# Kernel tuning notes

Hardware: AMD Instinct MI355X
Metric: run time of the kernel (lower is better)

Reference implementation:

```python
import jax, jax.numpy as jnp
import numpy as np

D_MODEL = 1024
N_HEADS = 16
SEQ = 2048
BATCH = 2
EPS = 1e-5


def layer_norm(x, g, b):
    mu = jnp.mean(x, axis=-1, keepdims=True)
    var = jnp.mean(jnp.square(x - mu), axis=-1, keepdims=True)
    return (x - mu) * jax.lax.rsqrt(var + EPS) * g + b


def setup_inputs() -> dict:
    key = jax.random.key(0)
    ks = jax.random.split(key, 10)
    D = D_MODEL
    s = lambda fan_in: 1.0 / np.sqrt(fan_in)
    return {
        "x": jax.random.normal(ks[0], (BATCH, SEQ, D), dtype=jnp.float32),
        # weights stored [in, out] (torch Linear is y = x @ W.T; equivalent math)
        "w_attn": jax.random.uniform(ks[1], (D, 3 * D), minval=-s(D), maxval=s(D), dtype=jnp.float32),
        "b_attn": jnp.zeros((3 * D,), jnp.float32),
        "w_proj": jax.random.uniform(ks[2], (D, D), minval=-s(D), maxval=s(D), dtype=jnp.float32),
        "b_proj": jnp.zeros((D,), jnp.float32),
        "ln1_g": jnp.ones((D,), jnp.float32),
        "ln1_b": jnp.zeros((D,), jnp.float32),
        "ln2_g": jnp.ones((D,), jnp.float32),
        "ln2_b": jnp.zeros((D,), jnp.float32),
        "w_fc1": jax.random.uniform(ks[3], (D, 4 * D), minval=-s(D), maxval=s(D), dtype=jnp.float32),
        "b_fc1": jnp.zeros((4 * D,), jnp.float32),
        "w_fc2": jax.random.uniform(ks[4], (4 * D, D), minval=-s(4 * D), maxval=s(4 * D), dtype=jnp.float32),
        "b_fc2": jnp.zeros((D,), jnp.float32),
    }


def reference(x, w_attn, b_attn, w_proj, b_proj, ln1_g, ln1_b, ln2_g, ln2_b, w_fc1, b_fc1, w_fc2, b_fc2):
    B, L, D = x.shape
    H = N_HEADS
    Dh = D // H

    # --- attention sublayer ---
    h = layer_norm(x, ln1_g, ln1_b)
    qkv = h @ w_attn + b_attn                      # [B, L, 3D]
    # SOURCE BUG (faithful): q, k, v are all taken from the k third.
    k = qkv[..., D:2 * D]
    kh = k.reshape(B, L, H, Dh).transpose(0, 2, 1, 3)   # [B, H, L, Dh]
    att = jnp.einsum('bhqd,bhkd->bhqk', kh, kh) / jnp.sqrt(jnp.float32(Dh))
    att = jax.nn.softmax(att, axis=-1)
    out = jnp.einsum('bhqk,bhkd->bhqd', att, kh)         # [B, H, L, Dh]
    out = out.transpose(0, 2, 1, 3).reshape(B, L, D)
    x = x + (out @ w_proj + b_proj)

    # --- feed-forward sublayer ---
    h = layer_norm(x, ln2_g, ln2_b)
    h = jax.nn.relu(h @ w_fc1 + b_fc1)
    x = x + (h @ w_fc2 + b_fc2)
    return x
```

## Files before the change

kernel.cpp:

```cpp
#include <hip/hip_runtime.h>


typedef __attribute__((ext_vector_type(8))) short s8v;
typedef __attribute__((ext_vector_type(4))) short s4v;
typedef __attribute__((ext_vector_type(4))) float f4v;

#define D_MODEL 1024
#define SEQ 2048
#define BATCH 2
#define NH 16
#define DH 64
#define MROWS (BATCH * SEQ)

#define KH_SCALE 0.42466088f
#define KH_ISCALE 2.3548200f

__device__ __forceinline__ float b2f(unsigned short u) {
  union { unsigned int i; float f; } v; v.i = ((unsigned int)u) << 16; return v.f;
}
__device__ __forceinline__ unsigned short f2b(float f) {
  unsigned int i = __builtin_bit_cast(unsigned int, f);
  unsigned int r = (i + 0x7fffu + ((i >> 16) & 1u)) >> 16;
  return (unsigned short)r;
}
__device__ __forceinline__ void async16(const void* g, void* l) {
  __builtin_amdgcn_global_load_lds(
      (const __attribute__((address_space(1))) unsigned int*)g,
      (__attribute__((address_space(3))) unsigned int*)l, 16, 0, 0);
}
__device__ __forceinline__ unsigned short cvt_b(float f) { return f2b(f); }
__device__ __forceinline__ unsigned short cvt_b(unsigned short u) { return u; }

__device__ __forceinline__ float xp2(float x) {
#if __has_builtin(__builtin_amdgcn_exp2f)
  return __builtin_amdgcn_exp2f(x);
#else
  return exp2f(x);
#endif
}

__device__ __forceinline__ s4v cvt4(float a, float b, float c, float d) {
  unsigned int lo, hi;
  asm("v_cvt_pk_bf16_f32 %0, %1, %2" : "=v"(lo) : "v"(a), "v"(b));
  asm("v_cvt_pk_bf16_f32 %0, %1, %2" : "=v"(hi) : "v"(c), "v"(d));
  union { unsigned long long u; s4v v; } u;
  u.u = ((unsigned long long)hi << 32) | (unsigned long long)lo;
  return u.v;
}

#if __has_builtin(__builtin_amdgcn_mfma_f32_16x16x16_bf16)
__device__ __forceinline__ f4v mfma16(s4v a, s4v b, f4v c) {
  return __builtin_amdgcn_mfma_f32_16x16x16_bf16(a, b, c, 0, 0, 0);
}
#elif __has_builtin(__builtin_amdgcn_mfma_f32_16x16x16bf16_1k)
__device__ __forceinline__ f4v mfma16(s4v a, s4v b, f4v c) {
  return __builtin_amdgcn_mfma_f32_16x16x16bf16_1k(a, b, c, 0, 0, 0);
}
#else
__device__ __forceinline__ f4v mfma16(s4v a, s4v b, f4v c) {
  s8v aa = {a[0], a[1], a[2], a[3], 0, 0, 0, 0};
  s8v bb = {b[0], b[1], b[2], b[3], 0, 0, 0, 0};
  return __builtin_amdgcn_mfma_f32_16x16x32_bf16(aa, bb, c, 0, 0, 0);
}
#endif

typedef __attribute__((address_space(3))) const unsigned short* lds_cp;
__device__ __forceinline__ s4v tr16(lds_cp p) {
  unsigned long long d;
  asm volatile("ds_read_b64_tr_b16 %0, %1" : "=v"(d) : "v"(p));
  return __builtin_bit_cast(s4v, d);
}

__device__ __forceinline__ int xcd_swz(int bidl, int nwg) {
  return (nwg & 7) ? bidl : ((bidl & 7) * (nwg >> 3) + (bidl >> 3));
}

__global__ __launch_bounds__(256) void ln_kernel(
    const float* __restrict__ x, const float* __restrict__ g,
    const float* __restrict__ bb, unsigned short* __restrict__ out) {
  int row = blockIdx.x;
  int t = threadIdx.x;
  const float* xr = x + (size_t)row * D_MODEL;
  float v[4];
  float s = 0.f, s2 = 0.f;
#pragma unroll
  for (int i = 0; i < 4; ++i) {
    float f = xr[t + 256 * i];
    v[i] = f; s += f; s2 += f * f;
  }
#pragma unroll
  for (int off = 1; off < 64; off <<= 1) {
    s += __shfl_xor(s, off, 64);
    s2 += __shfl_xor(s2, off, 64);
  }
  __shared__ float red[8];
  if ((t & 63) == 0) { red[t >> 6] = s; red[4 + (t >> 6)] = s2; }
  __syncthreads();
  s = red[0] + red[1] + red[2] + red[3];
  s2 = red[4] + red[5] + red[6] + red[7];
  float mu = s * (1.f / D_MODEL);
  float var = s2 * (1.f / D_MODEL) - mu * mu;
  float rstd = rsqrtf(var + 1e-5f);
#pragma unroll
  for (int i = 0; i < 4; ++i) {
    int c = t + 256 * i;
    float h = (v[i] - mu) * rstd * g[c] + bb[c];
    out[(size_t)row * D_MODEL + c] = f2b(h);
  }
}

template <typename T>
__global__ __launch_bounds__(256) void transpose_b(
    const T* __restrict__ src, unsigned short* __restrict__ dst,
    int srcStride, int dstStride, long long srcBatch, long long dstBatch) {
  __shared__ unsigned short tile[64][65];
  const T* s = src + (size_t)blockIdx.z * srcBatch;
  unsigned short* d = dst + (size_t)blockIdx.z * dstBatch;
  int n0 = blockIdx.x * 64, k0 = blockIdx.y * 64;
  for (int i = threadIdx.x; i < 4096; i += 256) {
    int k = i >> 6, n = i & 63;
    tile[k][n] = cvt_b(s[(size_t)(k0 + k) * srcStride + n0 + n]);
  }
  __syncthreads();
  for (int i = threadIdx.x; i < 4096; i += 256) {
    int n = i >> 6, k = i & 63;
    d[(size_t)(n0 + n) * dstStride + k0 + k] = tile[k][n];
  }
}

template <int RES, bool RELU, bool KH, int OUTF, int BM, int BN>
__global__ __launch_bounds__(256) void gemm_bt(
    const unsigned short* __restrict__ A, const unsigned short* __restrict__ Bt,
    const float* __restrict__ bias, const float* __restrict__ res,
    void* __restrict__ out, int M, int N, int K) {
  constexpr int MT = BM / 32;
  constexpr int NT = BN / 32;
  __shared__ __align__(16) unsigned short lsA[2][BM * 64];
  __shared__ __align__(16) unsigned short lsB[2][BN * 64];
  int tid = threadIdx.x;
  int lane = tid & 63, w = tid >> 6, quad = lane >> 4, l16 = lane & 15;
  int bidl = blockIdx.y * (int)gridDim.x + blockIdx.x;
  int swz = xcd_swz(bidl, (int)(gridDim.x * gridDim.y));
  int m0 = (swz / (int)gridDim.x) * BM, n0 = (swz % (int)gridDim.x) * BN;
  int wm = (w >> 1) * (BM / 2), wn = (w & 1) * (BN / 2);
  f4v acc[MT][NT] = {};

  auto stage = [&](int bsel, int ktE) {
#pragma unroll
    for (int i = 0; i < MT; ++i) {
      int cb = w * (BM * 2) + i * 64;
      int ci = cb + lane;
      int row = ci >> 3, c = ci & 7;
      int cs = c ^ (row & 7);
      async16(A + (size_t)(m0 + row) * K + ktE + cs * 8, &lsA[bsel][cb * 8]);
    }
#pragma unroll
    for (int i = 0; i < NT; ++i) {
      int cb = w * (BN * 2) + i * 64;
      int ci = cb + lane;
      int row = ci >> 3, c = ci & 7;
      int cs = c ^ (row & 7);
      async16(Bt + (size_t)(n0 + row) * K + ktE + cs * 8, &lsB[bsel][cb * 8]);
    }
  };

  stage(0, 0);
  int nK = K >> 6;
  for (int kt = 0; kt < nK; ++kt) {
    int b = kt & 1;
    if (kt + 1 < nK) {
      stage(b ^ 1, (kt + 1) << 6);
      if constexpr (MT + NT == 4)      asm volatile("s_waitcnt vmcnt(4)" ::: "memory");
      else if constexpr (MT + NT == 6) asm volatile("s_waitcnt vmcnt(6)" ::: "memory");
      else                             asm volatile("s_waitcnt vmcnt(8)" ::: "memory");
    } else {
      asm volatile("s_waitcnt vmcnt(0)" ::: "memory");
    }
    __builtin_amdgcn_sched_barrier(0);
    __builtin_amdgcn_s_barrier();
    __builtin_amdgcn_sched_barrier(0);
#pragma unroll
    for (int s = 0; s < 2; ++s) {
      s8v af[MT], bf[NT];
#pragma unroll
      for (int t = 0; t < MT; ++t) {
        int am = wm + t * 16 + l16;
        int ac = (s * 4 + quad) ^ (am & 7);
        af[t] = *(const s8v*)(&lsA[b][am * 64 + ac * 8]);
      }
#pragma unroll
      for (int t = 0; t < NT; ++t) {
        int bn = wn + t * 16 + l16;
        int bc = (s * 4 + quad) ^ (bn & 7);
        bf[t] = *(const s8v*)(&lsB[b][bn * 64 + bc * 8]);
      }
#pragma unroll
      for (int ti = 0; ti < MT; ++ti)
#pragma unroll
        for (int tj = 0; tj < NT; ++tj)
          acc[ti][tj] = __builtin_amdgcn_mfma_f32_16x16x32_bf16(
              af[ti], bf[tj], acc[ti][tj], 0, 0, 0);
    }
    asm volatile("s_waitcnt lgkmcnt(0)" ::: "memory");
    __builtin_amdgcn_sched_barrier(0);
    __builtin_amdgcn_s_barrier();
    __builtin_amdgcn_sched_barrier(0);
  }
#pragma unroll
  for (int tj = 0; tj < NT; ++tj) {
    int col = n0 + wn + tj * 16 + l16;
    float bv = bias[col];
#pragma unroll
    for (int ti = 0; ti < MT; ++ti) {
#pragma unroll
      for (int r = 0; r < 4; ++r) {
        int rowg = m0 + wm + ti * 16 + quad * 4 + r;
        float vv = acc[ti][tj][r] + bv;
        if (KH) vv *= KH_SCALE;
        if (RES == 2) vv += res[(size_t)rowg * N + col];
        if (RELU) vv = fmaxf(vv, 0.f);
        size_t oidx;
        if (KH) {
          int b2 = rowg >> 11, l = rowg & 2047, h = col >> 6, d = col & 63;
          oidx = (((size_t)(b2 * NH + h)) * SEQ + l) * DH + d;
        } else {
          oidx = (size_t)rowg * N + col;
        }
        if (OUTF == 0) ((unsigned short*)out)[oidx] = f2b(vv);
        else           ((float*)out)[oidx] = vv;
      }
    }
  }
}

__global__ __launch_bounds__(512, 2) void gemm256(
    const unsigned short* __restrict__ A, const unsigned short* __restrict__ Bt,
    const float* __restrict__ bias, unsigned short* __restrict__ out,
    bool relu, int M, int N, int K) {
  __shared__ __align__(16) unsigned short lsA[2][2][128 * 64];
  __shared__ __align__(16) unsigned short lsB[2][2][128 * 64];
  int tid = threadIdx.x;
  int lane = tid & 63, w = tid >> 6, quad = lane >> 4, l16 = lane & 15;
  int wr = w >> 2, wc = w & 3;
  int bidl = blockIdx.y * (int)gridDim.x + blockIdx.x;
  int swz = xcd_swz(bidl, (int)(gridDim.x * gridDim.y));
  int m0 = (swz / (int)gridDim.x) * 256, n0 = (swz % (int)gridDim.x) * 256;
  f4v acc[8][4] = {};
  s8v afh[2][4][2];
  s8v bfh[2][2][2];

  auto stageA = [&](int par, int h, int kt) {
#pragma unroll
    for (int i = 0; i < 2; ++i) {
      int cb = w * 128 + i * 64;
      int ci = cb + lane;
      int r = ci >> 3, c = ci & 7;
      int cs = c ^ (r & 7);
      int grow = ((r >> 6) << 7) + h * 64 + (r & 63);
      async16(A + (size_t)(m0 + grow) * K + kt * 64 + cs * 8,
              &lsA[par][h][cb * 8]);
    }
  };
  auto stageB = [&](int par, int h, int kt) {
#pragma unroll
    for (int i = 0; i < 2; ++i) {
      int cb = w * 128 + i * 64;
      int ci = cb + lane;
      int r = ci >> 3, c = ci & 7;
      int cs = c ^ (r & 7);
      int gn = ((r >> 5) << 6) + h * 32 + (r & 31);
      async16(Bt + (size_t)(n0 + gn) * K + kt * 64 + cs * 8,
              &lsB[par][h][cb * 8]);
    }
  };

#define PHASE(PAR, MH, NH, RA, RB, STAGE_STMT, VMN)                            \
  {                                                                            \
    if (RA) {                                                                  \
      _Pragma("unroll") for (int tm = 0; tm < 4; ++tm) {                       \
        int lr = wr * 64 + tm * 16 + l16;                                      \
        _Pragma("unroll") for (int s = 0; s < 2; ++s) {                        \
          int ac = (s * 4 + quad) ^ (lr & 7);                                  \
          afh[MH][tm][s] = *(const s8v*)(&lsA[PAR][MH][lr * 64 + ac * 8]);     \
        }                                                                      \
      }                                                                        \
    }                                                                          \
    if (RB) {                                                                  \
      _Pragma("unroll") for (int tn = 0; tn < 2; ++tn) {                       \
        int rb = wc * 32 + tn * 16 + l16;                                      \
        _Pragma("unroll") for (int s = 0; s < 2; ++s) {                        \
          int bc = (s * 4 + quad) ^ (rb & 7);                                  \
          bfh[NH][tn][s] = *(const s8v*)(&lsB[PAR][NH][rb * 64 + bc * 8]);     \
        }                                                                      \
      }                                                                        \
    }                                                                          \
    STAGE_STMT;                                                                \
    __builtin_amdgcn_sched_barrier(0);                                         \
    __builtin_amdgcn_s_barrier();                                              \
    __builtin_amdgcn_sched_barrier(0);                                         \
    __builtin_amdgcn_s_setprio(1);                                             \
    _Pragma("unroll") for (int s = 0; s < 2; ++s)                              \
      _Pragma("unroll") for (int tm = 0; tm < 4; ++tm)                         \
        _Pragma("unroll") for (int tn = 0; tn < 2; ++tn)                       \
          acc[MH * 4 + tm][NH * 2 + tn] =                                      \
              __builtin_amdgcn_mfma_f32_16x16x32_bf16(                         \
                  afh[MH][tm][s], bfh[NH][tn][s],                              \
                  acc[MH * 4 + tm][NH * 2 + tn], 0, 0, 0);                     \
    __builtin_amdgcn_s_setprio(0);                                             \
    __builtin_amdgcn_sched_barrier(0);                                         \
    if (VMN == 4) { asm volatile("s_waitcnt vmcnt(4)" ::: "memory"); }         \
    else if (VMN == 0) { asm volatile("s_waitcnt vmcnt(0)" ::: "memory"); }    \
    __builtin_amdgcn_sched_barrier(0);                                         \
    __builtin_amdgcn_s_barrier();                                              \
    __builtin_amdgcn_sched_barrier(0);                                         \
  }

  int nT = K >> 6;
  stageA(0, 0, 0); stageB(0, 0, 0); stageA(0, 1, 0); stageB(0, 1, 0);
  stageB(1, 0, 1); stageA(1, 0, 1);
  asm volatile("s_waitcnt vmcnt(4)" ::: "memory");
  __builtin_amdgcn_sched_barrier(0);
  __builtin_amdgcn_s_barrier();
  __builtin_amdgcn_sched_barrier(0);

  for (int t = 0; t < nT; t += 2) {
    bool s2 = (t + 2) < nT, s3 = (t + 3) < nT;
    PHASE(0, 0, 0, 1, 1, { stageA(1, 1, t + 1); }, -1)
    PHASE(0, 1, 0, 1, 0, { stageB(1, 1, t + 1); }, -1)
    PHASE(0, 0, 1, 0, 1, { if (s2) stageB(0, 0, t + 2); }, -1)
    PHASE(0, 1, 1, 0, 0, { if (s2) stageA(0, 0, t + 2); }, (s2 ? 4 : 0))
    PHASE(1, 0, 0, 1, 1, { if (s2) stageA(0, 1, t + 2); }, -1)
    PHASE(1, 1, 0, 1, 0, { if (s2) stageB(0, 1, t + 2); }, -1)
    PHASE(1, 0, 1, 0, 1, { if (s3) stageB(1, 0, t + 3); }, -1)
    PHASE(1, 1, 1, 0, 0, { if (s3) stageA(1, 0, t + 3); }, (s3 ? 4 : 0))
  }
#undef PHASE

#pragma unroll
  for (int mi = 0; mi < 8; ++mi) {
    int mh = mi >> 2, tm = mi & 3;
#pragma unroll
    for (int nj = 0; nj < 4; ++nj) {
      int nh = nj >> 1, tn = nj & 1;
      int col = n0 + wc * 64 + nh * 32 + tn * 16 + l16;
      float bv = bias[col];
#pragma unroll
      for (int r = 0; r < 4; ++r) {
        int rowg = m0 + wr * 128 + mh * 64 + tm * 16 + quad * 4 + r;
        float vv = acc[mi][nj][r] + bv;
        if (relu) vv = fmaxf(vv, 0.f);
        out[(size_t)rowg * N + col] = f2b(vv);
      }
    }
  }
}

__global__ __launch_bounds__(256) void gemm_proj(
    const unsigned short* __restrict__ Opart, const float* __restrict__ lpart,
    const unsigned short* __restrict__ Bt, const float* __restrict__ bias,
    const float* __restrict__ res, float* __restrict__ out, int M, int N, int K) {
  __shared__ __align__(16) unsigned short lsA[2][64 * 64];
  __shared__ __align__(16) unsigned short lsB[2][64 * 64];
  int tid = threadIdx.x;
  int lane = tid & 63, w = tid >> 6, quad = lane >> 4, l16 = lane & 15;
  int bidl = blockIdx.y * (int)gridDim.x + blockIdx.x;
  int swz = xcd_swz(bidl, (int)(gridDim.x * gridDim.y));
  int m0 = (swz / (int)gridDim.x) * 64, n0 = (swz % (int)gridDim.x) * 64;
  int wm = (w >> 1) * 32, wn = (w & 1) * 32;
  f4v acc[2][2] = {};

  int ci_[2], csA[2], mA[2], b2A[2], lA[2];
#pragma unroll
  for (int i = 0; i < 2; ++i) {
    int cb = w * 128 + i * 64;
    int ci = cb + lane;
    int row = ci >> 3, c = ci & 7;
    ci_[i] = ci; csA[i] = c ^ (row & 7);
    mA[i] = m0 + row; b2A[i] = mA[i] >> 11; lA[i] = mA[i] & 2047;
  }
  s8v o0r[2], o1r[2];
  float lsr0[2], lsr1[2];
  auto issueA = [&](int kt) {
#pragma unroll
    for (int i = 0; i < 2; ++i) {
      const unsigned short* pa =
          Opart + (size_t)mA[i] * D_MODEL + kt * 64 + csA[i] * 8;
      o0r[i] = *(const s8v*)pa;
      o1r[i] = *(const s8v*)(pa + (size_t)MROWS * D_MODEL);
      size_t lidx = ((size_t)b2A[i] * NH + kt) * SEQ + lA[i];
      lsr0[i] = lpart[lidx];
      lsr1[i] = lpart[(size_t)BATCH * NH * SEQ + lidx];
    }
  };
  auto issueB = [&](int bsel, int ktE) {
#pragma unroll
    for (int i = 0; i < 2; ++i) {
      int cb = w * 128 + i * 64;
      int ci = cb + lane;
      int row = ci >> 3, c = ci & 7;
      int cs = c ^ (row & 7);
      async16(Bt + (size_t)(n0 + row) * K + ktE + cs * 8, &lsB[bsel][cb * 8]);
    }
  };
  auto combineWrite = [&](int bsel) {
#pragma unroll
    for (int i = 0; i < 2; ++i) {
      float inv = KH_ISCALE / (lsr0[i] + lsr1[i]);
      float f[8];
#pragma unroll
      for (int j = 0; j < 8; ++j)
        f[j] = (b2f((unsigned short)o0r[i][j]) +
                b2f((unsigned short)o1r[i][j])) * inv;
      s4v lo = cvt4(f[0], f[1], f[2], f[3]);
      s4v hi = cvt4(f[4], f[5], f[6], f[7]);
      s8v vv = {lo[0], lo[1], lo[2], lo[3], hi[0], hi[1], hi[2], hi[3]};
      *(s8v*)(&lsA[bsel][ci_[i] * 8]) = vv;
    }
  };

  issueA(0); issueB(0, 0);
  __builtin_amdgcn_sched_barrier(0);
  asm volatile("s_waitcnt vmcnt(2)" ::: "memory");
  __builtin_amdgcn_sched_barrier(0);
  combineWrite(0);
  asm volatile("s_waitcnt lgkmcnt(0)" ::: "memory");
  __builtin_amdgcn_sched_barrier(0);

  int nK = K >> 6;
  for (int kt = 0; kt < nK; ++kt) {
    int b = kt & 1;
    if (kt + 1 < nK) {
      issueA(kt + 1); issueB(b ^ 1, (kt + 1) << 6);
      __builtin_amdgcn_sched_barrier(0);
      asm volatile("s_waitcnt vmcnt(10)" ::: "memory");
    } else {
      __builtin_amdgcn_sched_barrier(0);
      asm volatile("s_waitcnt vmcnt(0)" ::: "memory");
    }
    __builtin_amdgcn_sched_barrier(0);
    __builtin_amdgcn_s_barrier();
    __builtin_amdgcn_sched_barrier(0);
#pragma unroll
    for (int s = 0; s < 2; ++s) {
      s8v af[2], bf[2];
#pragma unroll
      for (int t = 0; t < 2; ++t) {
        int am = wm + t * 16 + l16;
        int ac = (s * 4 + quad) ^ (am & 7);
        af[t] = *(const s8v*)(&lsA[b][am * 64 + ac * 8]);
      }
#pragma unroll
      for (int t = 0; t < 2; ++t) {
        int bn = wn + t * 16 + l16;
        int bc = (s * 4 + quad) ^ (bn & 7);
        bf[t] = *(const s8v*)(&lsB[b][bn * 64 + bc * 8]);
      }
#pragma unroll
      for (int ti = 0; ti < 2; ++ti)
#pragma unroll
        for (int tj = 0; tj < 2; ++tj)
          acc[ti][tj] = __builtin_amdgcn_mfma_f32_16x16x32_bf16(
              af[ti], bf[tj], acc[ti][tj], 0, 0, 0);
    }
    if (kt + 1 < nK) {
      __builtin_amdgcn_sched_barrier(0);
      asm volatile("s_waitcnt vmcnt(2)" ::: "memory");
      __builtin_amdgcn_sched_barrier(0);
      combineWrite(b ^ 1);
    }
    asm volatile("s_waitcnt lgkmcnt(0)" ::: "memory");
    __builtin_amdgcn_sched_barrier(0);
    __builtin_amdgcn_s_barrier();
    __builtin_amdgcn_sched_barrier(0);
  }
#pragma unroll
  for (int tj = 0; tj < 2; ++tj) {
    int col = n0 + wn + tj * 16 + l16;
    float bv = bias[col];
#pragma unroll
    for (int ti = 0; ti < 2; ++ti) {
#pragma unroll
      for (int r = 0; r < 4; ++r) {
        int rowg = m0 + wm + ti * 16 + quad * 4 + r;
        float vv = acc[ti][tj][r] + bv + res[(size_t)rowg * N + col];
        out[(size_t)rowg * N + col] = vv;
      }
    }
  }
}

__global__ __launch_bounds__(256) void flash_k(
    const unsigned short* __restrict__ kh,
    unsigned short* __restrict__ Opart, float* __restrict__ lpart) {
  __shared__ __align__(16) unsigned short lsK[2][8192];
  int tid = threadIdx.x;
  int lane = tid & 63, w = tid >> 6, quad = lane >> 4, l16 = lane & 15;
  int split = blockIdx.x, bh = blockIdx.y, qb = blockIdx.z;
  const unsigned short* khB = kh + (size_t)bh * SEQ * DH;
  unsigned short* Op = Opart + (size_t)split * MROWS * D_MODEL;
  float* lp = lpart + (size_t)split * BATCH * NH * SEQ;
  s8v aQ[2][2];
#pragma unroll
  for (int g = 0; g < 2; ++g) {
    int q = qb * 128 + w * 32 + g * 16 + l16;
#pragma unroll
    for (int s = 0; s < 2; ++s)
      aQ[g][s] = *(const s8v*)(khB + (size_t)q * DH + s * 32 + quad * 8);
  }
  const s8v vone8 = {(short)0x3F80, (short)0x3F80, (short)0x3F80, (short)0x3F80,
                     (short)0x3F80, (short)0x3F80, (short)0x3F80, (short)0x3F80};
  f4v accO[2][4] = {};
  f4v accL[2] = {};

  auto stageK = [&](int bsel, int key0) {
#pragma unroll
    for (int i = 0; i < 4; ++i) {
      int ci = w * 256 + i * 64 + lane;
      async16(khB + (size_t)(key0 + ((ci >> 1) & 127)) * DH +
                  (ci >> 8) * 16 + (ci & 1) * 8,
              &lsK[bsel][(w * 256 + i * 64) * 8]);
    }
  };
  lds_cp ls0 = (lds_cp)&lsK[0][0];
  lds_cp trb = ls0 + quad * 64 + l16 * 4;

  stageK(0, split * 1024);
  for (int kt8 = 0; kt8 < 8; ++kt8) {
    int b = kt8 & 1;
    if (kt8 + 1 < 8) {
      stageK(b ^ 1, split * 1024 + (kt8 + 1) * 128);
      asm volatile("s_waitcnt vmcnt(4)" ::: "memory");
    } else {
      asm volatile("s_waitcnt vmcnt(0)" ::: "memory");
    }
    __builtin_amdgcn_sched_barrier(0);
    __builtin_amdgcn_s_barrier();
    __builtin_amdgcn_sched_barrier(0);
#pragma unroll
    for (int half = 0; half < 2; ++half) {
      f4v accST[2][4] = {};
#pragma unroll
      for (int s = 0; s < 2; ++s) {
#pragma unroll
        for (int tj = 0; tj < 4; ++tj) {
          s8v kf = *(const s8v*)(&lsK[b][(2 * s + (quad >> 1)) * 2048 +
                                         (half * 64 + tj * 16 + l16) * 16 +
                                         (quad & 1) * 8]);
#pragma unroll
          for (int g = 0; g < 2; ++g)
            accST[g][tj] = __builtin_amdgcn_mfma_f32_16x16x32_bf16(
                kf, aQ[g][s], accST[g][tj], 0, 0, 0);
        }
      }
      s4v pprev[2];
#pragma unroll
      for (int tj = 0; tj < 4; ++tj) {
        s4v vt[4];
#pragma unroll
        for (int db = 0; db < 4; ++db)
          vt[db] = tr16(trb + b * 8192 + db * 2048 + half * 1024 + tj * 256);
        s4v pf[2];
#pragma unroll
        for (int g = 0; g < 2; ++g) {
          float p0 = xp2(accST[g][tj][0]);
          float p1 = xp2(accST[g][tj][1]);
          float p2 = xp2(accST[g][tj][2]);
          float p3 = xp2(accST[g][tj][3]);
          pf[g] = cvt4(p0, p1, p2, p3);
        }
        if (tj & 1) {
#pragma unroll
          for (int g = 0; g < 2; ++g) {
            s8v pp = {pprev[g][0], pprev[g][1], pprev[g][2], pprev[g][3],
                      pf[g][0], pf[g][1], pf[g][2], pf[g][3]};
            accL[g] = __builtin_amdgcn_mfma_f32_16x16x32_bf16(
                pp, vone8, accL[g], 0, 0, 0);
          }
        } else {
#pragma unroll
          for (int g = 0; g < 2; ++g) pprev[g] = pf[g];
        }
        asm volatile("s_waitcnt lgkmcnt(0)" ::: "memory");
        __builtin_amdgcn_sched_barrier(0);
#pragma unroll
        for (int db = 0; db < 4; ++db)
#pragma unroll
          for (int g = 0; g < 2; ++g)
            accO[g][db] = mfma16(pf[g], vt[db], accO[g][db]);
      }
    }
    asm volatile("s_waitcnt lgkmcnt(0)" ::: "memory");
    __builtin_amdgcn_sched_barrier(0);
    __builtin_amdgcn_s_barrier();
    __builtin_amdgcn_sched_barrier(0);
  }
  int b = bh >> 4, h = bh & 15;
#pragma unroll
  for (int g = 0; g < 2; ++g) {
    if (l16 == 0) {
#pragma unroll
      for (int r = 0; r < 4; ++r) {
        int q = qb * 128 + w * 32 + g * 16 + quad * 4 + r;
        lp[(size_t)bh * SEQ + q] = accL[g][r];
      }
    }
#pragma unroll
    for (int r = 0; r < 4; ++r) {
      int l = qb * 128 + w * 32 + g * 16 + quad * 4 + r;
#pragma unroll
      for (int db = 0; db < 4; ++db) {
        int d = db * 16 + l16;
        Op[((size_t)(b * SEQ + l)) * D_MODEL + h * DH + d] = f2b(accO[g][db][r]);
      }
    }
  }
}

extern "C" void kernel_launch(void* const* d_in, const int* in_sizes, int n_in,
                              void* d_out, int out_size, void* d_ws, size_t ws_size,
                              hipStream_t stream) {
  (void)in_sizes; (void)n_in; (void)out_size;
  const float* x      = (const float*)d_in[0];
  const float* w_attn = (const float*)d_in[1];
  const float* b_attn = (const float*)d_in[2];
  const float* w_proj = (const float*)d_in[3];
  const float* b_proj = (const float*)d_in[4];
  const float* ln1_g  = (const float*)d_in[5];
  const float* ln1_b  = (const float*)d_in[6];
  const float* ln2_g  = (const float*)d_in[7];
  const float* ln2_b  = (const float*)d_in[8];
  const float* w_fc1  = (const float*)d_in[9];
  const float* b_fc1  = (const float*)d_in[10];
  const float* w_fc2  = (const float*)d_in[11];
  const float* b_fc2  = (const float*)d_in[12];

  char* ws = (char*)d_ws;
  unsigned short* Opart = (unsigned short*)ws;
  unsigned short* kh    = (unsigned short*)(ws + (size_t)(16u << 20));
  float*          x1    = (float*)(ws + (size_t)(32u << 20));
  unsigned short* hbuf  = (unsigned short*)(ws + (size_t)(48u << 20));
  float*          lpart = (float*)(ws + (size_t)(48u << 20));
  float* outf = (float*)d_out;
  bool big_ws = ws_size >= ((size_t)72u << 20);

  unsigned short* wTk;
  unsigned short* wTp;
  unsigned short* wTf1;
  unsigned short* wTf2;
  unsigned short* fc1o;
  if (big_ws) {
    wTk  = (unsigned short*)(ws + (size_t)(56u << 20));
    wTp  = wTk;
    wTf1 = wTk;
    wTf2 = (unsigned short*)(ws + (size_t)(64u << 20));
    fc1o = (unsigned short*)ws;
  } else {
    wTk  = (unsigned short*)ws;
    wTp  = (unsigned short*)(ws + (size_t)(24u << 20));
    wTf1 = (unsigned short*)ws;
    wTf2 = (unsigned short*)(ws + (size_t)(8u << 20));
    fc1o = kh;
  }

  dim3 blk(256);
  hipLaunchKernelGGL(ln_kernel, dim3(MROWS), blk, 0, stream, x, ln1_g, ln1_b, hbuf);
  hipLaunchKernelGGL(transpose_b<float>, dim3(16, 16, 1), blk, 0, stream,
                     w_attn + 1024, wTk, 3 * D_MODEL, D_MODEL, 0LL, 0LL);
  hipLaunchKernelGGL((gemm_bt<0, false, true, 0, 64, 64>), dim3(16, 64), blk, 0,
                     stream, hbuf, wTk, b_attn + 1024, nullptr, (void*)kh,
                     MROWS, D_MODEL, D_MODEL);
  hipLaunchKernelGGL(flash_k, dim3(2, 32, SEQ / 128), blk, 0, stream,
                     kh, Opart, lpart);
  hipLaunchKernelGGL(transpose_b<float>, dim3(16, 16, 1), blk, 0, stream,
                     w_proj, wTp, D_MODEL, D_MODEL, 0LL, 0LL);
  hipLaunchKernelGGL(gemm_proj, dim3(16, 64), blk, 0, stream,
                     Opart, lpart, wTp, b_proj, x, x1,
                     MROWS, D_MODEL, D_MODEL);
  hipLaunchKernelGGL(ln_kernel, dim3(MROWS), blk, 0, stream, x1, ln2_g, ln2_b, hbuf);
  hipLaunchKernelGGL(transpose_b<float>, dim3(64, 16, 1), blk, 0, stream,
                     w_fc1, wTf1, 4 * D_MODEL, D_MODEL, 0LL, 0LL);
  hipLaunchKernelGGL(transpose_b<float>, dim3(16, 64, 1), blk, 0, stream,
                     w_fc2, wTf2, D_MODEL, 4 * D_MODEL, 0LL, 0LL);
  if (big_ws) {
    hipLaunchKernelGGL(gemm256, dim3(16, 16), dim3(512), 0, stream,
                       hbuf, wTf1, b_fc1, fc1o, true,
                       MROWS, 4 * D_MODEL, D_MODEL);
    hipLaunchKernelGGL((gemm_bt<2, false, false, 1, 64, 64>), dim3(16, 64), blk, 0,
                       stream, fc1o, wTf2, b_fc2, x1, (void*)outf,
                       MROWS, D_MODEL, 4 * D_MODEL);
  } else {
    for (int c = 0; c < 2; ++c) {
      const unsigned short* h2c = hbuf + (size_t)c * 2048 * D_MODEL;
      const float* x1c = x1 + (size_t)c * 2048 * D_MODEL;
      float* outc = outf + (size_t)c * 2048 * D_MODEL;
      hipLaunchKernelGGL((gemm_bt<0, true, false, 0, 128, 64>), dim3(64, 16), blk, 0,
                         stream, h2c, wTf1, b_fc1, nullptr, (void*)fc1o,
                         2048, 4 * D_MODEL, D_MODEL);
      hipLaunchKernelGGL((gemm_bt<2, false, false, 1, 64, 64>), dim3(16, 32), blk, 0,
                         stream, fc1o, wTf2, b_fc2, x1c, (void*)outc,
                         2048, D_MODEL, 4 * D_MODEL);
    }
  }
}
```

Baseline: 317.1 us.

## Add intra-block split-K GEMM with 512 threads for 64x64 tiles

Introduces gemm_bt2, a 64x64-tile GEMM where each block of 8 waves is split into two K-halves. Each half computes a partial 64x64 result, and the halves are reduced through shared memory before the fused epilogue. The kernel replaces the 64x64 gemm_bt for the K projection and for the FC2 GEMM. The goal is more waves per output tile for latency hiding on these small-tile GEMMs, at the cost of an extra shared-memory reduction and barrier, and a larger block that may limit occupancy.

```diff
diff --git a/kernel.cpp b/kernel.cpp
--- a/kernel.cpp
+++ b/kernel.cpp
@@ -228,6 +228,130 @@
         }
         if (OUTF == 0) ((unsigned short*)out)[oidx] = f2b(vv);
         else           ((float*)out)[oidx] = vv;
+      }
+    }
+  }
+}
+
+template <int RES, bool RELU, bool KH, int OUTF>
+__global__ __launch_bounds__(512) void gemm_bt2(
+    const unsigned short* __restrict__ A, const unsigned short* __restrict__ Bt,
+    const float* __restrict__ bias, const float* __restrict__ res,
+    void* __restrict__ out, int M, int N, int K) {
+  __shared__ __align__(16) unsigned short lsA[2][2][64 * 64];
+  __shared__ __align__(16) unsigned short lsB[2][2][64 * 64];
+  int tid = threadIdx.x;
+  int lane = tid & 63, w = tid >> 6, quad = lane >> 4, l16 = lane & 15;
+  int kg = w >> 2, wi = w & 3;
+  int bidl = blockIdx.y * (int)gridDim.x + blockIdx.x;
+  int swz = xcd_swz(bidl, (int)(gridDim.x * gridDim.y));
+  int m0 = (swz / (int)gridDim.x) * 64, n0 = (swz % (int)gridDim.x) * 64;
+  int wm = (wi >> 1) * 32, wn = (wi & 1) * 32;
+  f4v acc[2][2] = {};
+  int kbase = kg * (K >> 1);
+
+  auto stage = [&](int par, int ktE) {
+#pragma unroll
+    for (int i = 0; i < 2; ++i) {
+      int cb = wi * 128 + i * 64;
+      int ci = cb + lane;
+      int row = ci >> 3, c = ci & 7;
+      int cs = c ^ (row & 7);
+      async16(A + (size_t)(m0 + row) * K + kbase + ktE + cs * 8,
+              &lsA[kg][par][cb * 8]);
+    }
+#pragma unroll
+    for (int i = 0; i < 2; ++i) {
+      int cb = wi * 128 + i * 64;
+      int ci = cb + lane;
+      int row = ci >> 3, c = ci & 7;
+      int cs = c ^ (row & 7);
+      async16(Bt + (size_t)(n0 + row) * K + kbase + ktE + cs * 8,
+              &lsB[kg][par][cb * 8]);
+    }
+  };
+
+  stage(0, 0);
+  int nS = K >> 7;
+  for (int st = 0; st < nS; ++st) {
+    int par = st & 1;
+    if (st + 1 < nS) {
+      stage(par ^ 1, (st + 1) << 6);
+      asm volatile("s_waitcnt vmcnt(4)" ::: "memory");
+    } else {
+      asm volatile("s_waitcnt vmcnt(0)" ::: "memory");
+    }
+    __builtin_amdgcn_sched_barrier(0);
+    __builtin_amdgcn_s_barrier();
+    __builtin_amdgcn_sched_barrier(0);
+#pragma unroll
+    for (int s = 0; s < 2; ++s) {
+      s8v af[2], bf[2];
+#pragma unroll
+      for (int t = 0; t < 2; ++t) {
+        int am = wm + t * 16 + l16;
+        int ac = (s * 4 + quad) ^ (am & 7);
+        af[t] = *(const s8v*)(&lsA[kg][par][am * 64 + ac * 8]);
+      }
+#pragma unroll
+      for (int t = 0; t < 2; ++t) {
+        int bn = wn + t * 16 + l16;
+        int bc = (s * 4 + quad) ^ (bn & 7);
+        bf[t] = *(const s8v*)(&lsB[kg][par][bn * 64 + bc * 8]);
+      }
+#pragma unroll
+      for (int ti = 0; ti < 2; ++ti)
+#pragma unroll
+        for (int tj = 0; tj < 2; ++tj)
+          acc[ti][tj] = __builtin_amdgcn_mfma_f32_16x16x32_bf16(
+              af[ti], bf[tj], acc[ti][tj], 0, 0, 0);
+    }
+    asm volatile("s_waitcnt lgkmcnt(0)" ::: "memory");
+    __builtin_amdgcn_sched_barrier(0);
+    __builtin_amdgcn_s_barrier();
+    __builtin_amdgcn_sched_barrier(0);
+  }
+
+  float* red = (float*)&lsA[0][0][0];
+  if (kg == 1) {
+#pragma unroll
+    for (int tj = 0; tj < 2; ++tj)
+#pragma unroll
+      for (int ti = 0; ti < 2; ++ti)
+#pragma unroll
+        for (int r = 0; r < 4; ++r)
+          red[(wm + ti * 16 + quad * 4 + r) * 64 + wn + tj * 16 + l16] =
+              acc[ti][tj][r];
+  }
+  asm volatile("s_waitcnt lgkmcnt(0)" ::: "memory");
+  __builtin_amdgcn_sched_barrier(0);
+  __builtin_amdgcn_s_barrier();
+  __builtin_amdgcn_sched_barrier(0);
+  if (kg == 0) {
+#pragma unroll
+    for (int tj = 0; tj < 2; ++tj) {
+      int col = n0 + wn + tj * 16 + l16;
+      float bv = bias[col];
+#pragma unroll
+      for (int ti = 0; ti < 2; ++ti) {
+#pragma unroll
+        for (int r = 0; r < 4; ++r) {
+          int rowl = wm + ti * 16 + quad * 4 + r;
+          int rowg = m0 + rowl;
+          float vv = acc[ti][tj][r] + red[rowl * 64 + wn + tj * 16 + l16] + bv;
+          if (KH) vv *= KH_SCALE;
+          if (RES == 2) vv += res[(size_t)rowg * N + col];
+          if (RELU) vv = fmaxf(vv, 0.f);
+          size_t oidx;
+          if (KH) {
+            int b2 = rowg >> 11, l = rowg & 2047, h = col >> 6, d = col & 63;
+            oidx = (((size_t)(b2 * NH + h)) * SEQ + l) * DH + d;
+          } else {
+            oidx = (size_t)rowg * N + col;
+          }
+          if (OUTF == 0) ((unsigned short*)out)[oidx] = f2b(vv);
+          else           ((float*)out)[oidx] = vv;
+        }
       }
     }
   }
@@ -663,10 +787,11 @@
   }
 
   dim3 blk(256);
+  dim3 blk2(512);
   hipLaunchKernelGGL(ln_kernel, dim3(MROWS), blk, 0, stream, x, ln1_g, ln1_b, hbuf);
   hipLaunchKernelGGL(transpose_b<float>, dim3(16, 16, 1), blk, 0, stream,
                      w_attn + 1024, wTk, 3 * D_MODEL, D_MODEL, 0LL, 0LL);
-  hipLaunchKernelGGL((gemm_bt<0, false, true, 0, 64, 64>), dim3(16, 64), blk, 0,
+  hipLaunchKernelGGL((gemm_bt2<0, false, true, 0>), dim3(16, 64), blk2, 0,
                      stream, hbuf, wTk, b_attn + 1024, nullptr, (void*)kh,
                      MROWS, D_MODEL, D_MODEL);
   hipLaunchKernelGGL(flash_k, dim3(2, 32, SEQ / 128), blk, 0, stream,
@@ -685,7 +810,7 @@
     hipLaunchKernelGGL(gemm256, dim3(16, 16), dim3(512), 0, stream,
                        hbuf, wTf1, b_fc1, fc1o, true,
                        MROWS, 4 * D_MODEL, D_MODEL);
-    hipLaunchKernelGGL((gemm_bt<2, false, false, 1, 64, 64>), dim3(16, 64), blk, 0,
+    hipLaunchKernelGGL((gemm_bt2<2, false, false, 1>), dim3(16, 64), blk2, 0,
                        stream, fc1o, wTf2, b_fc2, x1, (void*)outf,
                        MROWS, D_MODEL, 4 * D_MODEL);
   } else {
@@ -696,7 +821,7 @@
       hipLaunchKernelGGL((gemm_bt<0, true, false, 0, 128, 64>), dim3(64, 16), blk, 0,
                          stream, h2c, wTf1, b_fc1, nullptr, (void*)fc1o,
                          2048, 4 * D_MODEL, D_MODEL);
-      hipLaunchKernelGGL((gemm_bt<2, false, false, 1, 64, 64>), dim3(16, 32), blk, 0,
+      hipLaunchKernelGGL((gemm_bt2<2, false, false, 1>), dim3(16, 32), blk2, 0,
                          stream, fc1o, wTf2, b_fc2, x1c, (void*)outc,
                          2048, D_MODEL, 4 * D_MODEL);
     }
```

New measurement: 325.9 us. +2.8%, slower.

## Add dedicated FC2 GEMM kernel with async A staging and register-resident B

Applied to the files above, without the earlier changes.

Replaces the generic templated GEMM used for the FC2 projection with a specialized 64x64-tile kernel. A tiles are double-buffered in shared memory through async global-to-LDS copies, while B fragments are loaded straight from global memory into registers. Explicit waitcnt and sched barriers overlap the next tile's loads with MFMA compute. This aims to cut LDS traffic and hide load latency on the long K=4096 loop, at the cost of uncoalesced per-lane B reads and more hand-tuned scheduling.

```diff
diff --git a/kernel.cpp b/kernel.cpp
--- a/kernel.cpp
+++ b/kernel.cpp
@@ -228,6 +228,119 @@
         }
         if (OUTF == 0) ((unsigned short*)out)[oidx] = f2b(vv);
         else           ((float*)out)[oidx] = vv;
+      }
+    }
+  }
+}
+
+__global__ __launch_bounds__(256) void gemm_fc2(
+    const unsigned short* __restrict__ A, const unsigned short* __restrict__ Bt,
+    const float* __restrict__ bias, const float* __restrict__ res,
+    float* __restrict__ out, int M, int N, int K) {
+  __shared__ __align__(16) unsigned short lsA[2][64 * 64];
+  int tid = threadIdx.x;
+  int lane = tid & 63, w = tid >> 6, quad = lane >> 4, l16 = lane & 15;
+  int bidl = blockIdx.y * (int)gridDim.x + blockIdx.x;
+  int swz = xcd_swz(bidl, (int)(gridDim.x * gridDim.y));
+  int m0 = (swz / (int)gridDim.x) * 64, n0 = (swz % (int)gridDim.x) * 64;
+  int wm = (w >> 1) * 32, wn = (w & 1) * 32;
+  f4v acc[2][2] = {};
+
+  const unsigned short* bp[2][2];
+#pragma unroll
+  for (int t = 0; t < 2; ++t)
+#pragma unroll
+    for (int s = 0; s < 2; ++s)
+      bp[t][s] = Bt + (size_t)(n0 + wn + t * 16 + l16) * K + (s * 4 + quad) * 8;
+
+  auto stageA = [&](int bsel, int ktE) {
+#pragma unroll
+    for (int i = 0; i < 2; ++i) {
+      int cb = w * 128 + i * 64;
+      int ci = cb + lane;
+      int row = ci >> 3, c = ci & 7;
+      int cs = c ^ (row & 7);
+      async16(A + (size_t)(m0 + row) * K + ktE + cs * 8, &lsA[bsel][cb * 8]);
+    }
+  };
+  auto loadB = [&](s8v (&bR)[2][2], int kt) {
+#pragma unroll
+    for (int t = 0; t < 2; ++t)
+#pragma unroll
+      for (int s = 0; s < 2; ++s)
+        bR[t][s] = *(const s8v*)(bp[t][s] + (size_t)kt * 64);
+  };
+  auto compute = [&](int bsel, const s8v (&bR)[2][2]) {
+#pragma unroll
+    for (int s = 0; s < 2; ++s) {
+      s8v af[2];
+#pragma unroll
+      for (int t = 0; t < 2; ++t) {
+        int am = wm + t * 16 + l16;
+        int ac = (s * 4 + quad) ^ (am & 7);
+        af[t] = *(const s8v*)(&lsA[bsel][am * 64 + ac * 8]);
+      }
+#pragma unroll
+      for (int ti = 0; ti < 2; ++ti)
+#pragma unroll
+        for (int tj = 0; tj < 2; ++tj)
+          acc[ti][tj] = __builtin_amdgcn_mfma_f32_16x16x32_bf16(
+              af[ti], bR[tj][s], acc[ti][tj], 0, 0, 0);
+    }
+  };
+
+  s8v bR0[2][2], bR1[2][2];
+  stageA(0, 0);
+  loadB(bR0, 0);
+  int nK = K >> 6;
+  for (int kt = 0; kt < nK; kt += 2) {
+    if (kt + 1 < nK) {
+      stageA(1, (kt + 1) << 6);
+      loadB(bR1, kt + 1);
+      __builtin_amdgcn_sched_barrier(0);
+      asm volatile("s_waitcnt vmcnt(6)" ::: "memory");
+    } else {
+      __builtin_amdgcn_sched_barrier(0);
+      asm volatile("s_waitcnt vmcnt(0)" ::: "memory");
+    }
+    __builtin_amdgcn_sched_barrier(0);
+    __builtin_amdgcn_s_barrier();
+    __builtin_amdgcn_sched_barrier(0);
+    compute(0, bR0);
+    asm volatile("s_waitcnt lgkmcnt(0)" ::: "memory");
+    __builtin_amdgcn_sched_barrier(0);
+    __builtin_amdgcn_s_barrier();
+    __builtin_amdgcn_sched_barrier(0);
+    if (kt + 1 >= nK) break;
+    if (kt + 2 < nK) {
+      stageA(0, (kt + 2) << 6);
+      loadB(bR0, kt + 2);
+      __builtin_amdgcn_sched_barrier(0);
+      asm volatile("s_waitcnt vmcnt(6)" ::: "memory");
+    } else {
+      __builtin_amdgcn_sched_barrier(0);
+      asm volatile("s_waitcnt vmcnt(0)" ::: "memory");
+    }
+    __builtin_amdgcn_sched_barrier(0);
+    __builtin_amdgcn_s_barrier();
+    __builtin_amdgcn_sched_barrier(0);
+    compute(1, bR1);
+    asm volatile("s_waitcnt lgkmcnt(0)" ::: "memory");
+    __builtin_amdgcn_sched_barrier(0);
+    __builtin_amdgcn_s_barrier();
+    __builtin_amdgcn_sched_barrier(0);
+  }
+#pragma unroll
+  for (int tj = 0; tj < 2; ++tj) {
+    int col = n0 + wn + tj * 16 + l16;
+    float bv = bias[col];
+#pragma unroll
+    for (int ti = 0; ti < 2; ++ti) {
+#pragma unroll
+      for (int r = 0; r < 4; ++r) {
+        int rowg = m0 + wm + ti * 16 + quad * 4 + r;
+        float vv = acc[ti][tj][r] + bv + res[(size_t)rowg * N + col];
+        out[(size_t)rowg * N + col] = vv;
       }
     }
   }
@@ -685,8 +798,8 @@
     hipLaunchKernelGGL(gemm256, dim3(16, 16), dim3(512), 0, stream,
                        hbuf, wTf1, b_fc1, fc1o, true,
                        MROWS, 4 * D_MODEL, D_MODEL);
-    hipLaunchKernelGGL((gemm_bt<2, false, false, 1, 64, 64>), dim3(16, 64), blk, 0,
-                       stream, fc1o, wTf2, b_fc2, x1, (void*)outf,
+    hipLaunchKernelGGL(gemm_fc2, dim3(16, 64), blk, 0, stream,
+                       fc1o, wTf2, b_fc2, x1, outf,
                        MROWS, D_MODEL, 4 * D_MODEL);
   } else {
     for (int c = 0; c < 2; ++c) {
@@ -696,8 +809,8 @@
       hipLaunchKernelGGL((gemm_bt<0, true, false, 0, 128, 64>), dim3(64, 16), blk, 0,
                          stream, h2c, wTf1, b_fc1, nullptr, (void*)fc1o,
                          2048, 4 * D_MODEL, D_MODEL);
-      hipLaunchKernelGGL((gemm_bt<2, false, false, 1, 64, 64>), dim3(16, 32), blk, 0,
-                         stream, fc1o, wTf2, b_fc2, x1c, (void*)outc,
+      hipLaunchKernelGGL(gemm_fc2, dim3(16, 32), blk, 0, stream,
+                         fc1o, wTf2, b_fc2, x1c, outc,
                          2048, D_MODEL, 4 * D_MODEL);
     }
   }
```

After: 399.1 us. 1.26x slower.

## Drop split-K flash attention and normalize output inside flash kernel

Applied to the files above, without the earlier changes.

Removes the two-way key split in the flash attention kernel. Each block now iterates over all 16 key tiles and normalizes its output by the softmax denominator before writing bf16 directly into a buffer aliased to d_out. The projection GEMM then reuses the generic gemm_bt kernel instead of a custom kernel that combined the two partials. This avoids writing and reading two partial outputs plus the lse arrays, at the cost of half as many flash blocks (512 instead of 1024) and twice as long a serial loop per block.

```diff
diff --git a/kernel.cpp b/kernel.cpp
--- a/kernel.cpp
+++ b/kernel.cpp
@@ -355,150 +355,13 @@
   }
 }
 
-__global__ __launch_bounds__(256) void gemm_proj(
-    const unsigned short* __restrict__ Opart, const float* __restrict__ lpart,
-    const unsigned short* __restrict__ Bt, const float* __restrict__ bias,
-    const float* __restrict__ res, float* __restrict__ out, int M, int N, int K) {
-  __shared__ __align__(16) unsigned short lsA[2][64 * 64];
-  __shared__ __align__(16) unsigned short lsB[2][64 * 64];
-  int tid = threadIdx.x;
-  int lane = tid & 63, w = tid >> 6, quad = lane >> 4, l16 = lane & 15;
-  int bidl = blockIdx.y * (int)gridDim.x + blockIdx.x;
-  int swz = xcd_swz(bidl, (int)(gridDim.x * gridDim.y));
-  int m0 = (swz / (int)gridDim.x) * 64, n0 = (swz % (int)gridDim.x) * 64;
-  int wm = (w >> 1) * 32, wn = (w & 1) * 32;
-  f4v acc[2][2] = {};
-
-  int ci_[2], csA[2], mA[2], b2A[2], lA[2];
-#pragma unroll
-  for (int i = 0; i < 2; ++i) {
-    int cb = w * 128 + i * 64;
-    int ci = cb + lane;
-    int row = ci >> 3, c = ci & 7;
-    ci_[i] = ci; csA[i] = c ^ (row & 7);
-    mA[i] = m0 + row; b2A[i] = mA[i] >> 11; lA[i] = mA[i] & 2047;
-  }
-  s8v o0r[2], o1r[2];
-  float lsr0[2], lsr1[2];
-  auto issueA = [&](int kt) {
-#pragma unroll
-    for (int i = 0; i < 2; ++i) {
-      const unsigned short* pa =
-          Opart + (size_t)mA[i] * D_MODEL + kt * 64 + csA[i] * 8;
-      o0r[i] = *(const s8v*)pa;
-      o1r[i] = *(const s8v*)(pa + (size_t)MROWS * D_MODEL);
-      size_t lidx = ((size_t)b2A[i] * NH + kt) * SEQ + lA[i];
-      lsr0[i] = lpart[lidx];
-      lsr1[i] = lpart[(size_t)BATCH * NH * SEQ + lidx];
-    }
-  };
-  auto issueB = [&](int bsel, int ktE) {
-#pragma unroll
-    for (int i = 0; i < 2; ++i) {
-      int cb = w * 128 + i * 64;
-      int ci = cb + lane;
-      int row = ci >> 3, c = ci & 7;
-      int cs = c ^ (row & 7);
-      async16(Bt + (size_t)(n0 + row) * K + ktE + cs * 8, &lsB[bsel][cb * 8]);
-    }
-  };
-  auto combineWrite = [&](int bsel) {
-#pragma unroll
-    for (int i = 0; i < 2; ++i) {
-      float inv = KH_ISCALE / (lsr0[i] + lsr1[i]);
-      float f[8];
-#pragma unroll
-      for (int j = 0; j < 8; ++j)
-        f[j] = (b2f((unsigned short)o0r[i][j]) +
-                b2f((unsigned short)o1r[i][j])) * inv;
-      s4v lo = cvt4(f[0], f[1], f[2], f[3]);
-      s4v hi = cvt4(f[4], f[5], f[6], f[7]);
-      s8v vv = {lo[0], lo[1], lo[2], lo[3], hi[0], hi[1], hi[2], hi[3]};
-      *(s8v*)(&lsA[bsel][ci_[i] * 8]) = vv;
-    }
-  };
-
-  issueA(0); issueB(0, 0);
-  __builtin_amdgcn_sched_barrier(0);
-  asm volatile("s_waitcnt vmcnt(2)" ::: "memory");
-  __builtin_amdgcn_sched_barrier(0);
-  combineWrite(0);
-  asm volatile("s_waitcnt lgkmcnt(0)" ::: "memory");
-  __builtin_amdgcn_sched_barrier(0);
-
-  int nK = K >> 6;
-  for (int kt = 0; kt < nK; ++kt) {
-    int b = kt & 1;
-    if (kt + 1 < nK) {
-      issueA(kt + 1); issueB(b ^ 1, (kt + 1) << 6);
-      __builtin_amdgcn_sched_barrier(0);
-      asm volatile("s_waitcnt vmcnt(10)" ::: "memory");
-    } else {
-      __builtin_amdgcn_sched_barrier(0);
-      asm volatile("s_waitcnt vmcnt(0)" ::: "memory");
-    }
-    __builtin_amdgcn_sched_barrier(0);
-    __builtin_amdgcn_s_barrier();
-    __builtin_amdgcn_sched_barrier(0);
-#pragma unroll
-    for (int s = 0; s < 2; ++s) {
-      s8v af[2], bf[2];
-#pragma unroll
-      for (int t = 0; t < 2; ++t) {
-        int am = wm + t * 16 + l16;
-        int ac = (s * 4 + quad) ^ (am & 7);
-        af[t] = *(const s8v*)(&lsA[b][am * 64 + ac * 8]);
-      }
-#pragma unroll
-      for (int t = 0; t < 2; ++t) {
-        int bn = wn + t * 16 + l16;
-        int bc = (s * 4 + quad) ^ (bn & 7);
-        bf[t] = *(const s8v*)(&lsB[b][bn * 64 + bc * 8]);
-      }
-#pragma unroll
-      for (int ti = 0; ti < 2; ++ti)
-#pragma unroll
-        for (int tj = 0; tj < 2; ++tj)
-          acc[ti][tj] = __builtin_amdgcn_mfma_f32_16x16x32_bf16(
-              af[ti], bf[tj], acc[ti][tj], 0, 0, 0);
-    }
-    if (kt + 1 < nK) {
-      __builtin_amdgcn_sched_barrier(0);
-      asm volatile("s_waitcnt vmcnt(2)" ::: "memory");
-      __builtin_amdgcn_sched_barrier(0);
-      combineWrite(b ^ 1);
-    }
-    asm volatile("s_waitcnt lgkmcnt(0)" ::: "memory");
-    __builtin_amdgcn_sched_barrier(0);
-    __builtin_amdgcn_s_barrier();
-    __builtin_amdgcn_sched_barrier(0);
-  }
-#pragma unroll
-  for (int tj = 0; tj < 2; ++tj) {
-    int col = n0 + wn + tj * 16 + l16;
-    float bv = bias[col];
-#pragma unroll
-    for (int ti = 0; ti < 2; ++ti) {
-#pragma unroll
-      for (int r = 0; r < 4; ++r) {
-        int rowg = m0 + wm + ti * 16 + quad * 4 + r;
-        float vv = acc[ti][tj][r] + bv + res[(size_t)rowg * N + col];
-        out[(size_t)rowg * N + col] = vv;
-      }
-    }
-  }
-}
-
 __global__ __launch_bounds__(256) void flash_k(
-    const unsigned short* __restrict__ kh,
-    unsigned short* __restrict__ Opart, float* __restrict__ lpart) {
+    const unsigned short* __restrict__ kh, unsigned short* __restrict__ attn) {
   __shared__ __align__(16) unsigned short lsK[2][8192];
   int tid = threadIdx.x;
   int lane = tid & 63, w = tid >> 6, quad = lane >> 4, l16 = lane & 15;
-  int split = blockIdx.x, bh = blockIdx.y, qb = blockIdx.z;
+  int bh = blockIdx.x, qb = blockIdx.y;
   const unsigned short* khB = kh + (size_t)bh * SEQ * DH;
-  unsigned short* Op = Opart + (size_t)split * MROWS * D_MODEL;
-  float* lp = lpart + (size_t)split * BATCH * NH * SEQ;
   s8v aQ[2][2];
 #pragma unroll
   for (int g = 0; g < 2; ++g) {
@@ -524,11 +387,11 @@
   lds_cp ls0 = (lds_cp)&lsK[0][0];
   lds_cp trb = ls0 + quad * 64 + l16 * 4;
 
-  stageK(0, split * 1024);
-  for (int kt8 = 0; kt8 < 8; ++kt8) {
+  stageK(0, 0);
+  for (int kt8 = 0; kt8 < 16; ++kt8) {
     int b = kt8 & 1;
-    if (kt8 + 1 < 8) {
-      stageK(b ^ 1, split * 1024 + (kt8 + 1) * 128);
+    if (kt8 + 1 < 16) {
+      stageK(b ^ 1, (kt8 + 1) * 128);
       asm volatile("s_waitcnt vmcnt(4)" ::: "memory");
     } else {
       asm volatile("s_waitcnt vmcnt(0)" ::: "memory");
@@ -597,20 +460,15 @@
   int b = bh >> 4, h = bh & 15;
 #pragma unroll
   for (int g = 0; g < 2; ++g) {
-    if (l16 == 0) {
-#pragma unroll
-      for (int r = 0; r < 4; ++r) {
-        int q = qb * 128 + w * 32 + g * 16 + quad * 4 + r;
-        lp[(size_t)bh * SEQ + q] = accL[g][r];
-      }
-    }
 #pragma unroll
     for (int r = 0; r < 4; ++r) {
+      float inv = KH_ISCALE / accL[g][r];
       int l = qb * 128 + w * 32 + g * 16 + quad * 4 + r;
 #pragma unroll
       for (int db = 0; db < 4; ++db) {
         int d = db * 16 + l16;
-        Op[((size_t)(b * SEQ + l)) * D_MODEL + h * DH + d] = f2b(accO[g][db][r]);
+        attn[((size_t)(b * SEQ + l)) * D_MODEL + h * DH + d] =
+            f2b(accO[g][db][r] * inv);
       }
     }
   }
@@ -635,11 +493,10 @@
   const float* b_fc2  = (const float*)d_in[12];
 
   char* ws = (char*)d_ws;
-  unsigned short* Opart = (unsigned short*)ws;
   unsigned short* kh    = (unsigned short*)(ws + (size_t)(16u << 20));
   float*          x1    = (float*)(ws + (size_t)(32u << 20));
   unsigned short* hbuf  = (unsigned short*)(ws + (size_t)(48u << 20));
-  float*          lpart = (float*)(ws + (size_t)(48u << 20));
+  unsigned short* attn  = (unsigned short*)d_out;
   float* outf = (float*)d_out;
   bool big_ws = ws_size >= ((size_t)72u << 20);
 
@@ -669,12 +526,11 @@
   hipLaunchKernelGGL((gemm_bt<0, false, true, 0, 64, 64>), dim3(16, 64), blk, 0,
                      stream, hbuf, wTk, b_attn + 1024, nullptr, (void*)kh,
                      MROWS, D_MODEL, D_MODEL);
-  hipLaunchKernelGGL(flash_k, dim3(2, 32, SEQ / 128), blk, 0, stream,
-                     kh, Opart, lpart);
+  hipLaunchKernelGGL(flash_k, dim3(32, SEQ / 128), blk, 0, stream, kh, attn);
   hipLaunchKernelGGL(transpose_b<float>, dim3(16, 16, 1), blk, 0, stream,
                      w_proj, wTp, D_MODEL, D_MODEL, 0LL, 0LL);
-  hipLaunchKernelGGL(gemm_proj, dim3(16, 64), blk, 0, stream,
-                     Opart, lpart, wTp, b_proj, x, x1,
+  hipLaunchKernelGGL((gemm_bt<2, false, false, 1, 64, 64>), dim3(16, 64), blk, 0,
+                     stream, attn, wTp, b_proj, x, (void*)x1,
                      MROWS, D_MODEL, D_MODEL);
   hipLaunchKernelGGL(ln_kernel, dim3(MROWS), blk, 0, stream, x1, ln2_g, ln2_b, hbuf);
   hipLaunchKernelGGL(transpose_b<float>, dim3(64, 16, 1), blk, 0, stream,
```

New measurement: 308.1 us. -2.8%, faster.
